# Kernel optimization log

Measured on AMD Instinct MI355X. Metric: run time of the kernel, lower is better.

The kernel has to match this reference:

```python
import jax, jax.numpy as jnp
import numpy as np

TEMPERATURE = 8.0  # sqrt(d_k) with d_k = 64


def setup_inputs() -> dict:
    key = jax.random.key(0)
    kq, kk, kv, km = jax.random.split(key, 4)
    B, S, D = 32, 2048, 64
    q = jax.random.normal(kq, (B, S, D), dtype=jnp.float32)
    k = jax.random.normal(kk, (B, S, D), dtype=jnp.float32)
    v = jax.random.normal(kv, (B, S, D), dtype=jnp.float32)
    mask = jax.random.randint(km, (B, S, S), 0, 2).astype(jnp.bool_)
    return {"q": q, "k": k, "v": v, "mask": mask}


def reference(q, k, v, mask):
    # scores: [B, S, S] = q @ k^T, mask -> -inf, scale by 1/temperature
    scores = jnp.einsum("bqd,bkd->bqk", q, k)
    scores = jnp.where(mask, -jnp.inf, scores) / TEMPERATURE
    attn = jax.nn.softmax(scores, axis=2)
    output = jnp.einsum("bqk,bkd->bqd", attn, v)
    return (output, attn)
```

## Files before the change

kernel.cpp:

```cpp
#include <hip/hip_runtime.h>
#include <hip/hip_bf16.h>

typedef __attribute__((ext_vector_type(8))) short short8;
typedef __attribute__((ext_vector_type(4))) short short4b;
typedef __attribute__((ext_vector_type(4))) float f32x4;

#define S_LEN 2048
#define DIM   64
#define NB    32
#define BR    64
#define BC    64
#define NKT   (S_LEN / BC)

#define KP  72
#define BP  33
#define AP  68

__device__ __forceinline__ short f2bf(float f) {
    __hip_bfloat16 h = __float2bfloat16(f);
    return __builtin_bit_cast(short, h);
}


__global__ __launch_bounds__(256)
void conv_k_kernel(const float* __restrict__ k, short* __restrict__ kbf)
{
    size_t idx = ((size_t)blockIdx.x * 256 + threadIdx.x) * 8;
    const float* p = k + idx;
    float4 a = *(const float4*)p;
    float4 c = *(const float4*)(p + 4);
    short8 f;
    f[0]=f2bf(a.x); f[1]=f2bf(a.y); f[2]=f2bf(a.z); f[3]=f2bf(a.w);
    f[4]=f2bf(c.x); f[5]=f2bf(c.y); f[6]=f2bf(c.z); f[7]=f2bf(c.w);
    *(short8*)(kbf + idx) = f;
}

__global__ __launch_bounds__(256)
void conv_vt_kernel(const float* __restrict__ v, short* __restrict__ vtb)
{
    __shared__ float tile[64][65];
    const int t  = threadIdx.x;
    const int b  = blockIdx.x >> 5;
    const int j0 = (blockIdx.x & 31) * 64;

    #pragma unroll
    for (int p = 0; p < 4; ++p) {
        int j = (t >> 4) + p * 16;
        int d = (t & 15) * 4;
        float4 x = *(const float4*)(v + ((size_t)(b * S_LEN + j0 + j) * DIM + d));
        tile[j][d+0]=x.x; tile[j][d+1]=x.y; tile[j][d+2]=x.z; tile[j][d+3]=x.w;
    }
    __syncthreads();
    #pragma unroll
    for (int p = 0; p < 4; ++p) {
        int d  = (t >> 4) + p * 16;
        int j4 = (t & 15) * 4;
        short4b s4;
        s4[0]=f2bf(tile[j4+0][d]); s4[1]=f2bf(tile[j4+1][d]);
        s4[2]=f2bf(tile[j4+2][d]); s4[3]=f2bf(tile[j4+3][d]);
        *(short4b*)(vtb + ((size_t)(b * DIM + d) * S_LEN + j0 + j4)) = s4;
    }
}


__global__ __launch_bounds__(256, 4)
void sdpa_pf(const float* __restrict__ q, const int* __restrict__ mask,
             const short* __restrict__ kbf, const short* __restrict__ vtb,
             float* __restrict__ out, float* __restrict__ attn)
{
    __shared__ __align__(16) short Klds[BR * KP];
    __shared__ __align__(16) short Vtlds[DIM * KP];
    __shared__ __align__(16) float Albs[BR * AP];

    const int t  = threadIdx.x;
    const int l  = t & 63;
    const int wv = t >> 6;
    const int lg = l >> 4;
    const int ll = l & 15;

    const int bx  = blockIdx.x;
    const int kk  = bx >> 3;
    const int b   = (bx & 7) * 4 + (kk >> 5);
    const int i0  = (kk & 31) * BR;

    const float LOG2E_T = 0.18033688011112042f;

    const int krow = t >> 2;
    const int kcol = (t & 3) * 16;
    const size_t kgbase = (size_t)(b * S_LEN + krow) * DIM + kcol;
    const size_t vgbase = (size_t)(b * DIM + krow) * S_LEN + kcol;
    const size_t mbase  = (size_t)(b * S_LEN + i0 + 16 * wv) * S_LEN + l;

    short8 qf[2];
    {
        const float* qrow = q + ((size_t)(b * S_LEN + i0 + 16 * wv + ll) * DIM);
        #pragma unroll
        for (int s = 0; s < 2; ++s) {
            const float* p = qrow + s * 32 + lg * 8;
            float4 a = *(const float4*)p;
            float4 c = *(const float4*)(p + 4);
            short8 f;
            f[0]=f2bf(a.x); f[1]=f2bf(a.y); f[2]=f2bf(a.z); f[3]=f2bf(a.w);
            f[4]=f2bf(c.x); f[5]=f2bf(c.y); f[6]=f2bf(c.z); f[7]=f2bf(c.w);
            qf[s] = f;
        }
    }

    int mreg[16];
    #pragma unroll
    for (int r = 0; r < 16; ++r)
        mreg[r] = __builtin_nontemporal_load(mask + mbase + (size_t)r * S_LEN);
    short8 kr0 = *(const short8*)(kbf + kgbase);
    short8 kr1 = *(const short8*)(kbf + kgbase + 8);

    float rs[4] = {0.f, 0.f, 0.f, 0.f};
    unsigned long long w8[8];

    for (int o = 0; o < 4; ++o) {
        #pragma unroll
        for (int u = 0; u < 8; ++u) {
            const int kt = 8 * o + u;

            unsigned long long wb[4];
            #pragma unroll
            for (int r = 0; r < 16; ++r) {
                unsigned long long bal = __ballot(mreg[r] != 0);
                if ((r >> 2) == lg) wb[r & 3] = bal;
                if (lg == o && ll == r) w8[u] = bal;
            }

            const int ktn = (kt < NKT - 1) ? kt + 1 : kt;
            {
                const int* mrow = mask + mbase + (size_t)ktn * BC;
                #pragma unroll
                for (int r = 0; r < 16; ++r)
                    mreg[r] = __builtin_nontemporal_load(mrow + (size_t)r * S_LEN);
            }

            __syncthreads();
            {
                short* kd = &Klds[krow * KP + kcol];
                *(short8*)kd = kr0;
                *(short8*)(kd + 8) = kr1;
            }
            {
                const short* kb = kbf + kgbase + (size_t)ktn * BC * DIM;
                kr0 = *(const short8*)kb;
                kr1 = *(const short8*)(kb + 8);
            }
            __syncthreads();

            #pragma unroll
            for (int jt = 0; jt < 4; ++jt) {
                short8 b0 = *(short8*)&Klds[(jt * 16 + ll) * KP + lg * 8];
                short8 b1 = *(short8*)&Klds[(jt * 16 + ll) * KP + 32 + lg * 8];
                f32x4 c = {0.f, 0.f, 0.f, 0.f};
                c = __builtin_amdgcn_mfma_f32_16x16x32_bf16(qf[0], b0, c, 0, 0, 0);
                c = __builtin_amdgcn_mfma_f32_16x16x32_bf16(qf[1], b1, c, 0, 0, 0);
                #pragma unroll
                for (int r = 0; r < 4; ++r) {
                    unsigned int bit = (unsigned int)(wb[r] >> (jt * 16 + ll)) & 1u;
                    rs[r] += bit ? 0.f : __builtin_amdgcn_exp2f(c[r] * LOG2E_T);
                }
            }
        }
    }

    kr0 = *(const short8*)(kbf + kgbase);
    kr1 = *(const short8*)(kbf + kgbase + 8);
    short8 vr0 = *(const short8*)(vtb + vgbase);
    short8 vr1 = *(const short8*)(vtb + vgbase + 8);

    float inv[4];
    #pragma unroll
    for (int r = 0; r < 4; ++r) {
        float s = rs[r];
        s += __shfl_xor(s, 1);
        s += __shfl_xor(s, 2);
        s += __shfl_xor(s, 4);
        s += __shfl_xor(s, 8);
        inv[r] = 1.0f / s;
    }

    f32x4 oacc[4];
    #pragma unroll
    for (int dt = 0; dt < 4; ++dt) oacc[dt] = (f32x4){0.f, 0.f, 0.f, 0.f};

    float* const abase = attn + (size_t)b * S_LEN * S_LEN;

    for (int o = 0; o < 4; ++o) {
        #pragma unroll
        for (int u = 0; u < 8; ++u) {
            const int kt = 8 * o + u;
            const int j0 = kt * BC;

            unsigned long long wb[4];
            #pragma unroll
            for (int r = 0; r < 4; ++r)
                wb[r] = __shfl(w8[u], 16 * o + lg * 4 + r);

            __syncthreads();
            {
                short* kd = &Klds[krow * KP + kcol];
                *(short8*)kd = kr0;
                *(short8*)(kd + 8) = kr1;
                short* vd = &Vtlds[krow * KP + kcol];
                *(short8*)vd = vr0;
                *(short8*)(vd + 8) = vr1;
            }
            {
                const int ktn = (kt < NKT - 1) ? kt + 1 : kt;
                const short* kb = kbf + kgbase + (size_t)ktn * BC * DIM;
                kr0 = *(const short8*)kb;
                kr1 = *(const short8*)(kb + 8);
                const short* vb = vtb + vgbase + (size_t)ktn * BC;
                vr0 = *(const short8*)vb;
                vr1 = *(const short8*)(vb + 8);
            }
            __syncthreads();

            #pragma unroll
            for (int jt = 0; jt < 4; ++jt) {
                short8 b0 = *(short8*)&Klds[(jt * 16 + ll) * KP + lg * 8];
                short8 b1 = *(short8*)&Klds[(jt * 16 + ll) * KP + 32 + lg * 8];
                f32x4 c = {0.f, 0.f, 0.f, 0.f};
                c = __builtin_amdgcn_mfma_f32_16x16x32_bf16(qf[0], b0, c, 0, 0, 0);
                c = __builtin_amdgcn_mfma_f32_16x16x32_bf16(qf[1], b1, c, 0, 0, 0);
                #pragma unroll
                for (int r = 0; r < 4; ++r) {
                    unsigned int bit = (unsigned int)(wb[r] >> (jt * 16 + ll)) & 1u;
                    float pexp = bit ? 0.f : __builtin_amdgcn_exp2f(c[r] * LOG2E_T);
                    Albs[(16 * wv + lg * 4 + r) * AP + jt * 16 + ll] = pexp * inv[r];
                }
            }

            short8 paf[2];
            #pragma unroll
            for (int s = 0; s < 2; ++s) {
                const float* ap = &Albs[(16 * wv + ll) * AP + s * 32 + lg * 8];
                float4 x = *(const float4*)ap;
                float4 y = *(const float4*)(ap + 4);
                short8 f;
                f[0]=f2bf(x.x); f[1]=f2bf(x.y); f[2]=f2bf(x.z); f[3]=f2bf(x.w);
                f[4]=f2bf(y.x); f[5]=f2bf(y.y); f[6]=f2bf(y.z); f[7]=f2bf(y.w);
                paf[s] = f;
            }

            #pragma unroll
            for (int dt = 0; dt < 4; ++dt) {
                short8 b0 = *(short8*)&Vtlds[(dt * 16 + ll) * KP + lg * 8];
                short8 b1 = *(short8*)&Vtlds[(dt * 16 + ll) * KP + 32 + lg * 8];
                oacc[dt] = __builtin_amdgcn_mfma_f32_16x16x32_bf16(paf[0], b0, oacc[dt], 0, 0, 0);
                oacc[dt] = __builtin_amdgcn_mfma_f32_16x16x32_bf16(paf[1], b1, oacc[dt], 0, 0, 0);
            }

            #pragma unroll
            for (int ps = 0; ps < 4; ++ps) {
                int row = 16 * wv + lg + ps * 4;
                f32x4 val = *(f32x4*)&Albs[row * AP + ll * 4];
                float* dst = abase + (size_t)(i0 + row) * S_LEN + j0 + ll * 4;
                __builtin_nontemporal_store(val, (f32x4*)dst);
            }
        }
    }

    #pragma unroll
    for (int dt = 0; dt < 4; ++dt)
        #pragma unroll
        for (int r = 0; r < 4; ++r)
            out[(size_t)(b * S_LEN + i0 + 16 * wv + lg * 4 + r) * DIM + dt * 16 + ll] = oacc[dt][r];
}


__global__ __launch_bounds__(256, 3)
void sdpa_fb(const float* __restrict__ q, const float* __restrict__ k,
             const float* __restrict__ v, const int* __restrict__ mask,
             float* __restrict__ out, float* __restrict__ attn)
{
    __shared__ __align__(16) short Klds[BR * KP];
    __shared__ __align__(16) short Vtlds[DIM * KP];
    __shared__ __align__(16) unsigned long long Bits[BR * BP];
    __shared__ __align__(16) float Albs[BR * AP];

    const int t  = threadIdx.x;
    const int l  = t & 63;
    const int wv = t >> 6;
    const int lg = l >> 4;
    const int ll = l & 15;

    const int wg = blockIdx.x;
    const int b  = wg >> 5;
    const int i0 = (wg & 31) * BR;

    const float LOG2E_T = 0.18033688011112042f;

    short8 qf[2];
    {
        const float* qrow = q + ((size_t)(b * S_LEN + i0 + 16 * wv + ll) * DIM);
        #pragma unroll
        for (int s = 0; s < 2; ++s) {
            const float* p = qrow + s * 32 + lg * 8;
            float4 a = *(const float4*)p;
            float4 c = *(const float4*)(p + 4);
            short8 f;
            f[0]=f2bf(a.x); f[1]=f2bf(a.y); f[2]=f2bf(a.z); f[3]=f2bf(a.w);
            f[4]=f2bf(c.x); f[5]=f2bf(c.y); f[6]=f2bf(c.z); f[7]=f2bf(c.w);
            qf[s] = f;
        }
    }

    float rs[4] = {0.f, 0.f, 0.f, 0.f};

    for (int kt = 0; kt < NKT; ++kt) {
        const int j0 = kt * BC;
        #pragma unroll
        for (int p = 0; p < 4; ++p) {
            int row = (t >> 4) + p * 16;
            int dd  = (t & 15) * 4;
            float4 kv4 = *(const float4*)(k + ((size_t)(b * S_LEN + j0 + row) * DIM + dd));
            short4b s4;
            s4[0]=f2bf(kv4.x); s4[1]=f2bf(kv4.y); s4[2]=f2bf(kv4.z); s4[3]=f2bf(kv4.w);
            *(short4b*)&Klds[row * KP + dd] = s4;
        }
        {
            const int* mrow = mask + (size_t)(b * S_LEN + i0 + 16 * wv) * S_LEN + j0 + l;
            int mv[16];
            #pragma unroll
            for (int r = 0; r < 16; ++r)
                mv[r] = __builtin_nontemporal_load(mrow + (size_t)r * S_LEN);
            unsigned long long myword = 0ull;
            #pragma unroll
            for (int r = 0; r < 16; ++r) {
                unsigned long long bal = __ballot(mv[r] != 0);
                if (ll == r) myword = bal;
            }
            if (l < 16) Bits[(16 * wv + l) * BP + kt] = myword;
        }
        __syncthreads();

        unsigned long long wbits[4];
        #pragma unroll
        for (int r = 0; r < 4; ++r)
            wbits[r] = Bits[(16 * wv + lg * 4 + r) * BP + kt];

        #pragma unroll
        for (int jt = 0; jt < 4; ++jt) {
            short8 b0 = *(short8*)&Klds[(jt * 16 + ll) * KP + lg * 8];
            short8 b1 = *(short8*)&Klds[(jt * 16 + ll) * KP + 32 + lg * 8];
            f32x4 c = {0.f, 0.f, 0.f, 0.f};
            c = __builtin_amdgcn_mfma_f32_16x16x32_bf16(qf[0], b0, c, 0, 0, 0);
            c = __builtin_amdgcn_mfma_f32_16x16x32_bf16(qf[1], b1, c, 0, 0, 0);
            #pragma unroll
            for (int r = 0; r < 4; ++r) {
                unsigned int bit = (unsigned int)(wbits[r] >> (jt * 16 + ll)) & 1u;
                rs[r] += bit ? 0.f : __builtin_amdgcn_exp2f(c[r] * LOG2E_T);
            }
        }
        __syncthreads();
    }

    float inv[4];
    #pragma unroll
    for (int r = 0; r < 4; ++r) {
        float s = rs[r];
        s += __shfl_xor(s, 1);
        s += __shfl_xor(s, 2);
        s += __shfl_xor(s, 4);
        s += __shfl_xor(s, 8);
        inv[r] = 1.0f / s;
    }

    f32x4 oacc[4];
    #pragma unroll
    for (int dt = 0; dt < 4; ++dt) oacc[dt] = (f32x4){0.f, 0.f, 0.f, 0.f};

    for (int kt = 0; kt < NKT; ++kt) {
        const int j0 = kt * BC;
        #pragma unroll
        for (int p = 0; p < 4; ++p) {
            int row = (t >> 4) + p * 16;
            int dd  = (t & 15) * 4;
            float4 kv4 = *(const float4*)(k + ((size_t)(b * S_LEN + j0 + row) * DIM + dd));
            short4b s4;
            s4[0]=f2bf(kv4.x); s4[1]=f2bf(kv4.y); s4[2]=f2bf(kv4.z); s4[3]=f2bf(kv4.w);
            *(short4b*)&Klds[row * KP + dd] = s4;
        }
        #pragma unroll
        for (int it = 0; it < 8; ++it) {
            int jp = (t >> 4) + (it & 1) * 16;
            int dd = (t & 15) + (it >> 1) * 16;
            const float* vp = v + ((size_t)(b * S_LEN + j0 + jp * 2) * DIM + dd);
            float v0 = vp[0];
            float v1 = vp[DIM];
            unsigned int pk = (unsigned int)(unsigned short)f2bf(v0) |
                              ((unsigned int)(unsigned short)f2bf(v1) << 16);
            *(unsigned int*)&Vtlds[dd * KP + jp * 2] = pk;
        }
        __syncthreads();

        unsigned long long wbits[4];
        #pragma unroll
        for (int r = 0; r < 4; ++r)
            wbits[r] = Bits[(16 * wv + lg * 4 + r) * BP + kt];

        #pragma unroll
        for (int jt = 0; jt < 4; ++jt) {
            short8 b0 = *(short8*)&Klds[(jt * 16 + ll) * KP + lg * 8];
            short8 b1 = *(short8*)&Klds[(jt * 16 + ll) * KP + 32 + lg * 8];
            f32x4 c = {0.f, 0.f, 0.f, 0.f};
            c = __builtin_amdgcn_mfma_f32_16x16x32_bf16(qf[0], b0, c, 0, 0, 0);
            c = __builtin_amdgcn_mfma_f32_16x16x32_bf16(qf[1], b1, c, 0, 0, 0);
            #pragma unroll
            for (int r = 0; r < 4; ++r) {
                unsigned int bit = (unsigned int)(wbits[r] >> (jt * 16 + ll)) & 1u;
                float pexp = bit ? 0.f : __builtin_amdgcn_exp2f(c[r] * LOG2E_T);
                Albs[(16 * wv + lg * 4 + r) * AP + jt * 16 + ll] = pexp * inv[r];
            }
        }

        short8 paf[2];
        #pragma unroll
        for (int s = 0; s < 2; ++s) {
            const float* ap = &Albs[(16 * wv + ll) * AP + s * 32 + lg * 8];
            float4 x = *(const float4*)ap;
            float4 y = *(const float4*)(ap + 4);
            short8 f;
            f[0]=f2bf(x.x); f[1]=f2bf(x.y); f[2]=f2bf(x.z); f[3]=f2bf(x.w);
            f[4]=f2bf(y.x); f[5]=f2bf(y.y); f[6]=f2bf(y.z); f[7]=f2bf(y.w);
            paf[s] = f;
        }

        #pragma unroll
        for (int dt = 0; dt < 4; ++dt) {
            short8 b0 = *(short8*)&Vtlds[(dt * 16 + ll) * KP + lg * 8];
            short8 b1 = *(short8*)&Vtlds[(dt * 16 + ll) * KP + 32 + lg * 8];
            oacc[dt] = __builtin_amdgcn_mfma_f32_16x16x32_bf16(paf[0], b0, oacc[dt], 0, 0, 0);
            oacc[dt] = __builtin_amdgcn_mfma_f32_16x16x32_bf16(paf[1], b1, oacc[dt], 0, 0, 0);
        }

        {
            float* abase = attn + (size_t)b * S_LEN * S_LEN;
            #pragma unroll
            for (int ps = 0; ps < 4; ++ps) {
                int row = 16 * wv + lg + ps * 4;
                f32x4 val = *(f32x4*)&Albs[row * AP + ll * 4];
                float* dst = abase + (size_t)(i0 + row) * S_LEN + j0 + ll * 4;
                __builtin_nontemporal_store(val, (f32x4*)dst);
            }
        }
        __syncthreads();
    }

    #pragma unroll
    for (int dt = 0; dt < 4; ++dt)
        #pragma unroll
        for (int r = 0; r < 4; ++r)
            out[(size_t)(b * S_LEN + i0 + 16 * wv + lg * 4 + r) * DIM + dt * 16 + ll] = oacc[dt][r];
}

extern "C" void kernel_launch(void* const* d_in, const int* in_sizes, int n_in,
                              void* d_out, int out_size, void* d_ws, size_t ws_size,
                              hipStream_t stream) {
    const float* q    = (const float*)d_in[0];
    const float* k    = (const float*)d_in[1];
    const float* v    = (const float*)d_in[2];
    const int*   mask = (const int*)d_in[3];
    float* out  = (float*)d_out;
    float* attn = out + (size_t)NB * S_LEN * DIM;

    const size_t nel = (size_t)NB * S_LEN * DIM;
    const size_t ws_needed = 2 * nel * sizeof(short);

    if (ws_size >= ws_needed) {
        short* kbf = (short*)d_ws;
        short* vtb = kbf + nel;
        conv_k_kernel<<<dim3(nel / (256 * 8)), dim3(256), 0, stream>>>(k, kbf);
        conv_vt_kernel<<<dim3(NB * 32), dim3(256), 0, stream>>>(v, vtb);
        sdpa_pf<<<dim3(NB * (S_LEN / BR)), dim3(256), 0, stream>>>(q, mask, kbf, vtb, out, attn);
    } else {
        sdpa_fb<<<dim3(NB * (S_LEN / BR)), dim3(256), 0, stream>>>(q, k, v, mask, out, attn);
    }
}
```

Before: 309.8 us.

## Double-buffer mask prefetch two tiles ahead and use raw barriers

Mask rows are now prefetched two key tiles ahead in ping-pong register buffers. This gives the nontemporal mask loads more time to land before the ballot consumes them. The __syncthreads calls are replaced with raw s_barrier plus explicit lgkmcnt waits and sched_barrier fences, so global loads for the next K/V tile are no longer drained at each barrier. The cost is 16 more mask registers per thread under a 4-wave occupancy bound, which could cause spills or lower occupancy. The hand-placed scheduling barriers also constrain the compiler.

After: 305.2 us. Within noise of the previous version (-1.5%).

```diff
diff --git a/kernel.cpp b/kernel.cpp
--- a/kernel.cpp
+++ b/kernel.cpp
@@ -19,6 +19,18 @@
 __device__ __forceinline__ short f2bf(float f) {
     __hip_bfloat16 h = __float2bfloat16(f);
     return __builtin_bit_cast(short, h);
+}
+
+__device__ __forceinline__ void barrier_raw() {
+    __builtin_amdgcn_sched_barrier(0);
+    __builtin_amdgcn_s_barrier();
+    __builtin_amdgcn_sched_barrier(0);
+}
+__device__ __forceinline__ void barrier_pub() {
+    __builtin_amdgcn_sched_barrier(0);
+    asm volatile("s_waitcnt lgkmcnt(0)" ::: "memory");
+    __builtin_amdgcn_s_barrier();
+    __builtin_amdgcn_sched_barrier(0);
 }
 
 
@@ -64,7 +76,7 @@
 
 
 __global__ __launch_bounds__(256, 4)
-void sdpa_pf(const float* __restrict__ q, const int* __restrict__ mask,
+void sdpa_v8(const float* __restrict__ q, const int* __restrict__ mask,
              const short* __restrict__ kbf, const short* __restrict__ vtb,
              float* __restrict__ out, float* __restrict__ attn)
 {
@@ -106,12 +118,15 @@
         }
     }
 
-    int mreg[16];
+    short8 kA0 = *(const short8*)(kbf + kgbase);
+    short8 kA1 = *(const short8*)(kbf + kgbase + 8);
+    int mA[16], mB[16];
     #pragma unroll
     for (int r = 0; r < 16; ++r)
-        mreg[r] = __builtin_nontemporal_load(mask + mbase + (size_t)r * S_LEN);
-    short8 kr0 = *(const short8*)(kbf + kgbase);
-    short8 kr1 = *(const short8*)(kbf + kgbase + 8);
+        mA[r] = __builtin_nontemporal_load(mask + mbase + (size_t)r * S_LEN);
+    #pragma unroll
+    for (int r = 0; r < 16; ++r)
+        mB[r] = __builtin_nontemporal_load(mask + mbase + BC + (size_t)r * S_LEN);
 
     float rs[4] = {0.f, 0.f, 0.f, 0.f};
     unsigned long long w8[8];
@@ -120,35 +135,36 @@
         #pragma unroll
         for (int u = 0; u < 8; ++u) {
             const int kt = 8 * o + u;
+            int (&cur)[16] = (u & 1) ? mB : mA;
 
             unsigned long long wb[4];
             #pragma unroll
             for (int r = 0; r < 16; ++r) {
-                unsigned long long bal = __ballot(mreg[r] != 0);
+                unsigned long long bal = __ballot(cur[r] != 0);
                 if ((r >> 2) == lg) wb[r & 3] = bal;
                 if (lg == o && ll == r) w8[u] = bal;
             }
 
-            const int ktn = (kt < NKT - 1) ? kt + 1 : kt;
+            barrier_raw();
             {
-                const int* mrow = mask + mbase + (size_t)ktn * BC;
+                short* kd = &Klds[krow * KP + kcol];
+                *(short8*)kd = kA0;
+                *(short8*)(kd + 8) = kA1;
+            }
+            barrier_pub();
+
+            {
+                const int ktn = (kt < NKT - 1) ? kt + 1 : kt;
+                const short* kb = kbf + kgbase + (size_t)ktn * BC * DIM;
+                kA0 = *(const short8*)kb;
+                kA1 = *(const short8*)(kb + 8);
+                const int kt2 = (kt < NKT - 2) ? kt + 2 : kt;
+                const int* mrow = mask + mbase + (size_t)kt2 * BC;
                 #pragma unroll
                 for (int r = 0; r < 16; ++r)
-                    mreg[r] = __builtin_nontemporal_load(mrow + (size_t)r * S_LEN);
-            }
-
-            __syncthreads();
-            {
-                short* kd = &Klds[krow * KP + kcol];
-                *(short8*)kd = kr0;
-                *(short8*)(kd + 8) = kr1;
-            }
-            {
-                const short* kb = kbf + kgbase + (size_t)ktn * BC * DIM;
-                kr0 = *(const short8*)kb;
-                kr1 = *(const short8*)(kb + 8);
-            }
-            __syncthreads();
+                    cur[r] = __builtin_nontemporal_load(mrow + (size_t)r * S_LEN);
+            }
+            __builtin_amdgcn_sched_barrier(0);
 
             #pragma unroll
             for (int jt = 0; jt < 4; ++jt) {
@@ -166,10 +182,10 @@
         }
     }
 
-    kr0 = *(const short8*)(kbf + kgbase);
-    kr1 = *(const short8*)(kbf + kgbase + 8);
-    short8 vr0 = *(const short8*)(vtb + vgbase);
-    short8 vr1 = *(const short8*)(vtb + vgbase + 8);
+    kA0 = *(const short8*)(kbf + kgbase);
+    kA1 = *(const short8*)(kbf + kgbase + 8);
+    short8 vA0 = *(const short8*)(vtb + vgbase);
+    short8 vA1 = *(const short8*)(vtb + vgbase + 8);
 
     float inv[4];
     #pragma unroll
@@ -194,30 +210,32 @@
             const int kt = 8 * o + u;
             const int j0 = kt * BC;
 
-            unsigned long long wb[4];
-            #pragma unroll
-            for (int r = 0; r < 4; ++r)
-                wb[r] = __shfl(w8[u], 16 * o + lg * 4 + r);
-
-            __syncthreads();
+            barrier_raw();
             {
                 short* kd = &Klds[krow * KP + kcol];
-                *(short8*)kd = kr0;
-                *(short8*)(kd + 8) = kr1;
+                *(short8*)kd = kA0;
+                *(short8*)(kd + 8) = kA1;
                 short* vd = &Vtlds[krow * KP + kcol];
-                *(short8*)vd = vr0;
-                *(short8*)(vd + 8) = vr1;
-            }
+                *(short8*)vd = vA0;
+                *(short8*)(vd + 8) = vA1;
+            }
+            barrier_pub();
+
             {
                 const int ktn = (kt < NKT - 1) ? kt + 1 : kt;
                 const short* kb = kbf + kgbase + (size_t)ktn * BC * DIM;
-                kr0 = *(const short8*)kb;
-                kr1 = *(const short8*)(kb + 8);
+                kA0 = *(const short8*)kb;
+                kA1 = *(const short8*)(kb + 8);
                 const short* vb = vtb + vgbase + (size_t)ktn * BC;
-                vr0 = *(const short8*)vb;
-                vr1 = *(const short8*)(vb + 8);
-            }
-            __syncthreads();
+                vA0 = *(const short8*)vb;
+                vA1 = *(const short8*)(vb + 8);
+            }
+            __builtin_amdgcn_sched_barrier(0);
+
+            unsigned long long wb[4];
+            #pragma unroll
+            for (int r = 0; r < 4; ++r)
+                wb[r] = __shfl(w8[u], 16 * o + lg * 4 + r);
 
             #pragma unroll
             for (int jt = 0; jt < 4; ++jt) {
@@ -476,7 +494,7 @@
         short* vtb = kbf + nel;
         conv_k_kernel<<<dim3(nel / (256 * 8)), dim3(256), 0, stream>>>(k, kbf);
         conv_vt_kernel<<<dim3(NB * 32), dim3(256), 0, stream>>>(v, vtb);
-        sdpa_pf<<<dim3(NB * (S_LEN / BR)), dim3(256), 0, stream>>>(q, mask, kbf, vtb, out, attn);
+        sdpa_v8<<<dim3(NB * (S_LEN / BR)), dim3(256), 0, stream>>>(q, mask, kbf, vtb, out, attn);
     } else {
         sdpa_fb<<<dim3(NB * (S_LEN / BR)), dim3(256), 0, stream>>>(q, k, v, mask, out, attn);
     }
```
